# Performance work log

Measured on AMD Instinct MI355X. Metric: run time of the kernel, lower is better.

## Reference

```python
import jax, jax.numpy as jnp
import numpy as np

ROWS, N = 2048, 32768  # kernel requires N = 8 tiles * 1024 threads * 4 (float4)

def setup_inputs() -> dict:
    key = jax.random.key(0)
    kx, km = jax.random.split(key)
    x = jax.random.normal(kx, (ROWS, N), dtype=jnp.float32)
    mask = jax.random.randint(km, (ROWS, N), 0, 2).astype(jnp.bool_)
    return {"x": x, "mask": mask}

def reference(x, mask):
    # Masked inclusive cumulative sum along dim=1: cumsum(where(mask, x, 0))
    return jnp.cumsum(jnp.where(mask, x, jnp.float32(0)), axis=1)
```

## Files before the change

### kernel.cpp

```cpp
#include <hip/hip_runtime.h>


#define ROWS    2048
#define NCOL    32768
#define THREADS 1024
#define TILES   8
#define NCHUNK  (THREADS * TILES)

__global__ __launch_bounds__(THREADS, 1) void masked_cumsum_kernel(
    const float* __restrict__ x,
    const int*   __restrict__ mask,
    float*       __restrict__ out)
{
    const int row = blockIdx.x;
    const size_t base = (size_t)row * NCOL;
    const float4* __restrict__ xrow = (const float4*)(x + base);
    const int4*   __restrict__ mrow = (const int4*)(mask + base);
    float4*       __restrict__ orow = (float4*)(out + base);

    const int tid  = threadIdx.x;
    const int lane = tid & 63;
    const int wave = tid >> 6;

    __shared__ float csum[NCHUNK + NCHUNK / 8];
    __shared__ float wtot[16];

    float4 xv[TILES];
    int4   mv[TILES];
    #pragma unroll
    for (int t = 0; t < TILES; ++t) {
        xv[t] = xrow[t * THREADS + tid];
        mv[t] = mrow[t * THREADS + tid];
    }

    float4 p[TILES];
    #pragma unroll
    for (int t = 0; t < TILES; ++t) {
        float a0 = mv[t].x ? xv[t].x : 0.0f;
        float a1 = mv[t].y ? xv[t].y : 0.0f;
        float a2 = mv[t].z ? xv[t].z : 0.0f;
        float a3 = mv[t].w ? xv[t].w : 0.0f;
        p[t].x = a0;
        p[t].y = p[t].x + a1;
        p[t].z = p[t].y + a2;
        p[t].w = p[t].z + a3;
        int c = t * THREADS + tid;
        csum[c + (c >> 3)] = p[t].w;
    }
    __syncthreads();

    float s[8];
    float run = 0.0f;
    #pragma unroll
    for (int k = 0; k < 8; ++k) {
        run += csum[tid * 9 + k];
        s[k] = run;
    }

    float sc = run;
    #pragma unroll
    for (int d = 1; d < 64; d <<= 1) {
        float o = __shfl_up(sc, d);
        if (lane >= d) sc += o;
    }
    if (lane == 63) wtot[wave] = sc;
    __syncthreads();

    float woff = 0.0f;
    #pragma unroll
    for (int w = 0; w < 16; ++w)
        woff += (w < wave) ? wtot[w] : 0.0f;

    const float thr_excl = woff + (sc - run);

    #pragma unroll
    for (int k = 0; k < 8; ++k)
        csum[tid * 9 + k] = thr_excl + (k ? s[k - 1] : 0.0f);
    __syncthreads();

    #pragma unroll
    for (int t = 0; t < TILES; ++t) {
        int c = t * THREADS + tid;
        float off = csum[c + (c >> 3)];
        orow[t * THREADS + tid] =
            make_float4(off + p[t].x, off + p[t].y, off + p[t].z, off + p[t].w);
    }
}

extern "C" void kernel_launch(void* const* d_in, const int* in_sizes, int n_in,
                              void* d_out, int out_size, void* d_ws, size_t ws_size,
                              hipStream_t stream) {
    const float* x    = (const float*)d_in[0];
    const int*   mask = (const int*)d_in[1];
    float*       out  = (float*)d_out;
    masked_cumsum_kernel<<<ROWS, THREADS, 0, stream>>>(x, mask, out);
}
```

Baseline: 572.6 us.

## Split rows into segments with decoupled lookback across smaller blocks

Each row is split into 8 segments of 4096 elements, each handled by a 256-thread block. Segments chain their prefix through per-row flag slots in workspace using atomic loads and stores with spin-waiting. Blocks are ordered so that all rows' segment k are launched before segment k+1. Outputs are written with nontemporal stores. This raises occupancy and memory-level parallelism compared with one 1024-thread block per row, at the cost of a memset, serial lookback latency, and reliance on block scheduling order to avoid deadlock.

```diff
diff --git a/kernel.cpp b/kernel.cpp
--- a/kernel.cpp
+++ b/kernel.cpp
@@ -3,34 +3,47 @@
 
 #define ROWS    2048
 #define NCOL    32768
-#define THREADS 1024
-#define TILES   8
-#define NCHUNK  (THREADS * TILES)
+#define THREADS 256
+#define TILES   4
+#define SEGLEN  (THREADS * TILES * 4)
+#define NSEG    (NCOL / SEGLEN)
+#define NCHK    (THREADS * TILES)
 
-__global__ __launch_bounds__(THREADS, 1) void masked_cumsum_kernel(
+static_assert(ROWS == 2048, "seg/row decode uses >>11");
+static_assert(NSEG * SEGLEN == NCOL, "exact tiling");
+
+typedef float floatx4 __attribute__((ext_vector_type(4)));
+static_assert(sizeof(floatx4) == sizeof(float4), "layout match");
+
+__global__ __launch_bounds__(THREADS, 8) void masked_cumsum_lookback(
     const float* __restrict__ x,
     const int*   __restrict__ mask,
-    float*       __restrict__ out)
+    float*       __restrict__ out,
+    unsigned long long* __restrict__ flags)
 {
-    const int row = blockIdx.x;
-    const size_t base = (size_t)row * NCOL;
-    const float4* __restrict__ xrow = (const float4*)(x + base);
-    const int4*   __restrict__ mrow = (const int4*)(mask + base);
-    float4*       __restrict__ orow = (float4*)(out + base);
+    const int bid = blockIdx.x;
+    const int seg = bid >> 11;
+    const int row = bid & (ROWS - 1);
+
+    const size_t base = (size_t)row * NCOL + (size_t)seg * SEGLEN;
+    const float4* __restrict__ xs = (const float4*)(x + base);
+    const int4*   __restrict__ ms = (const int4*)(mask + base);
+    floatx4*      __restrict__ os = (floatx4*)(out + base);
 
     const int tid  = threadIdx.x;
     const int lane = tid & 63;
     const int wave = tid >> 6;
 
-    __shared__ float csum[NCHUNK + NCHUNK / 8];
-    __shared__ float wtot[16];
+    __shared__ float csum[NCHK + NCHK / 8];
+    __shared__ float wtot[THREADS / 64];
+    __shared__ float rowoff;
 
     float4 xv[TILES];
     int4   mv[TILES];
     #pragma unroll
     for (int t = 0; t < TILES; ++t) {
-        xv[t] = xrow[t * THREADS + tid];
-        mv[t] = mrow[t * THREADS + tid];
+        xv[t] = xs[t * THREADS + tid];
+        mv[t] = ms[t * THREADS + tid];
     }
 
     float4 p[TILES];
@@ -49,11 +62,13 @@
     }
     __syncthreads();
 
-    float s[8];
+    float s[TILES];
     float run = 0.0f;
+    const int c0 = tid * TILES;
     #pragma unroll
-    for (int k = 0; k < 8; ++k) {
-        run += csum[tid * 9 + k];
+    for (int k = 0; k < TILES; ++k) {
+        int c = c0 + k;
+        run += csum[c + (c >> 3)];
         s[k] = run;
     }
 
@@ -68,22 +83,50 @@
 
     float woff = 0.0f;
     #pragma unroll
-    for (int w = 0; w < 16; ++w)
+    for (int w = 0; w < THREADS / 64; ++w)
         woff += (w < wave) ? wtot[w] : 0.0f;
 
     const float thr_excl = woff + (sc - run);
 
     #pragma unroll
-    for (int k = 0; k < 8; ++k)
-        csum[tid * 9 + k] = thr_excl + (k ? s[k - 1] : 0.0f);
+    for (int k = 0; k < TILES; ++k) {
+        int c = c0 + k;
+        csum[c + (c >> 3)] = thr_excl + (k ? s[k - 1] : 0.0f);
+    }
+
+    if (tid == 0) {
+        float agg = 0.0f;
+        #pragma unroll
+        for (int w = 0; w < THREADS / 64; ++w) agg += wtot[w];
+
+        float pre = 0.0f;
+        if (seg > 0) {
+            const unsigned long long* slot = flags + (size_t)(seg - 1) * ROWS + row;
+            unsigned long long v =
+                __hip_atomic_load(slot, __ATOMIC_RELAXED, __HIP_MEMORY_SCOPE_AGENT);
+            while (!(v >> 32)) {
+                __builtin_amdgcn_s_sleep(1);
+                v = __hip_atomic_load(slot, __ATOMIC_RELAXED, __HIP_MEMORY_SCOPE_AGENT);
+            }
+            pre = __uint_as_float((unsigned)v);
+        }
+        if (seg < NSEG - 1) {
+            unsigned long long pk =
+                (1ULL << 32) | (unsigned long long)__float_as_uint(pre + agg);
+            __hip_atomic_store(flags + (size_t)seg * ROWS + row, pk,
+                               __ATOMIC_RELAXED, __HIP_MEMORY_SCOPE_AGENT);
+        }
+        rowoff = pre;
+    }
     __syncthreads();
 
+    const float ro = rowoff;
     #pragma unroll
     for (int t = 0; t < TILES; ++t) {
         int c = t * THREADS + tid;
-        float off = csum[c + (c >> 3)];
-        orow[t * THREADS + tid] =
-            make_float4(off + p[t].x, off + p[t].y, off + p[t].z, off + p[t].w);
+        float off = csum[c + (c >> 3)] + ro;
+        floatx4 o = { off + p[t].x, off + p[t].y, off + p[t].z, off + p[t].w };
+        __builtin_nontemporal_store(o, &os[t * THREADS + tid]);
     }
 }
 
@@ -93,5 +136,10 @@
     const float* x    = (const float*)d_in[0];
     const int*   mask = (const int*)d_in[1];
     float*       out  = (float*)d_out;
-    masked_cumsum_kernel<<<ROWS, THREADS, 0, stream>>>(x, mask, out);
+    unsigned long long* flags = (unsigned long long*)d_ws;
+
+    (void)hipMemsetAsync(d_ws, 0,
+                         (size_t)NSEG * ROWS * sizeof(unsigned long long), stream);
+
+    masked_cumsum_lookback<<<ROWS * NSEG, THREADS, 0, stream>>>(x, mask, out, flags);
 }
```

After: 601.6 us. +5.1%, slower.
